# Kernel optimization log

Measured on AMD Instinct MI355X. Metric: run time of the kernel, lower is better.

The kernel has to match this reference:

```python
import jax, jax.numpy as jnp
import numpy as np

B, T, V, E, H, HD, L, K = 64, 512, 50000, 512, 512, 256, 2, 16
START, STOP, PAD = 13, 14, 15
NEG = -10000.0


def setup_inputs() -> dict:
    key = jax.random.key(0)
    ks = jax.random.split(key, 12)
    x = jax.random.randint(ks[0], (B, T), 0, V, dtype=jnp.int32)
    emb_table = jax.random.normal(ks[1], (V, E), jnp.float32) * 0.1
    w_ih = jax.random.normal(ks[2], (L, 2, 4 * HD, E), jnp.float32) * 0.05
    w_hh = jax.random.normal(ks[3], (L, 2, 4 * HD, HD), jnp.float32) * 0.05
    b_ih = jax.random.normal(ks[4], (L, 2, 4 * HD), jnp.float32) * 0.05
    b_hh = jax.random.normal(ks[5], (L, 2, 4 * HD), jnp.float32) * 0.05
    h0 = jax.random.normal(ks[6], (2 * L, B, HD), jnp.float32)
    c0 = jax.random.normal(ks[7], (2 * L, B, HD), jnp.float32)
    w_out = jax.random.normal(ks[8], (K, H), jnp.float32) * 0.05
    b_out = jax.random.normal(ks[9], (K,), jnp.float32) * 0.05
    t = jax.random.normal(ks[10], (K, K), jnp.float32)
    # replicate the in-place edits (order matters: pad overrides stop/start crossings)
    t = t.at[START, :].set(NEG)
    t = t.at[:, STOP].set(NEG)
    t = t.at[PAD, :].set(0.0)
    t = t.at[:, PAD].set(0.0)
    return {"x": x, "seq_len": T, "emb_table": emb_table, "w_ih": w_ih,
            "w_hh": w_hh, "b_ih": b_ih, "b_hh": b_hh, "h0": h0, "c0": c0,
            "w_out": w_out, "b_out": b_out, "transition": t}


def _lstm_dir(xs, h0, c0, Wih, Whh, b):
    # xs: [B, T, in]; single-direction LSTM, torch gate order (i, f, g, o)
    def step(carry, x_t):
        h, c = carry
        gates = x_t @ Wih.T + h @ Whh.T + b  # [B, 4*HD]
        i, f, g, o = jnp.split(gates, 4, axis=-1)
        c = jax.nn.sigmoid(f) * c + jax.nn.sigmoid(i) * jnp.tanh(g)
        h = jax.nn.sigmoid(o) * jnp.tanh(c)
        return (h, c), h
    _, hs = jax.lax.scan(step, (h0, c0), jnp.swapaxes(xs, 0, 1))  # [T, B, HD]
    return jnp.swapaxes(hs, 0, 1)


def _log_exp_sum(vec):
    # faithful to the original: per-row max over last dim, but sum of exp over ALL elements
    m = jnp.max(vec, axis=-1)
    return m + jnp.log(jnp.sum(jnp.exp(vec - m[..., None])))


def reference(x, seq_len, emb_table, w_ih, w_hh, b_ih, b_hh, h0, c0, w_out, b_out, transition):
    out = emb_table[x]  # [B, T, E]
    for l in range(L):
        fwd = _lstm_dir(out, h0[2 * l], c0[2 * l], w_ih[l, 0], w_hh[l, 0], b_ih[l, 0] + b_hh[l, 0])
        bwd = _lstm_dir(out[:, ::-1], h0[2 * l + 1], c0[2 * l + 1], w_ih[l, 1], w_hh[l, 1], b_ih[l, 1] + b_hh[l, 1])[:, ::-1]
        out = jnp.concatenate([fwd, bwd], axis=-1)  # [B, T, H]
    tag_scores = out @ w_out.T + b_out  # [B, T, K]

    # CRF forward algorithm (vectorized form of the nested time/tag loops)
    alpha0 = jnp.full((B, K), NEG, dtype=tag_scores.dtype).at[:, START].set(0.0)

    def crf_step(alpha, feat_t):  # feat_t: [B, K]
        vec = alpha[:, None, :] + feat_t[:, :, None] + transition[None, :, :]  # [B, Knext, Kprev]
        m = jnp.max(vec, axis=-1)  # [B, Knext]
        # original log_exp_sum sums exp over the whole [B, Kprev] slice per next_tag
        s = jnp.sum(jnp.exp(vec - m[..., None]), axis=(0, 2))  # [Knext]
        return m + jnp.log(s)[None, :], None

    alpha, _ = jax.lax.scan(crf_step, alpha0, jnp.swapaxes(tag_scores, 0, 1))
    terminal = alpha + transition[STOP][None, :]
    forward_score = _log_exp_sum(terminal)  # [B]
    return tag_scores, forward_score
```

## Files before the change

### kernel.cpp

```cpp
#include <hip/hip_runtime.h>

#define B_ 64
#define T_ 512
#define E_ 512
#define HD_ 256
#define H_ 512
#define K_ 16
#define NEG_ (-10000.0f)
#define START_ 13
#define STOP_ 14

typedef unsigned int u32;
using half8  = __attribute__((ext_vector_type(8))) _Float16;
using f32x4  = __attribute__((ext_vector_type(4))) float;
using half2v = __attribute__((ext_vector_type(2))) _Float16;

__device__ __forceinline__ int dot4i8(u32 a, u32 b, int c) {
#if __has_builtin(__builtin_amdgcn_sdot4)
    return __builtin_amdgcn_sdot4((int)a, (int)b, c, false);
#else
    int r = c;
#pragma unroll
    for (int i = 0; i < 4; ++i) {
        int xa = ((int)a << (24 - 8 * i)) >> 24;
        int xb = ((int)b << (24 - 8 * i)) >> 24;
        r += xa * xb;
    }
    return r;
#endif
}
__device__ __forceinline__ int dotq(uint4 w, uint4 h, int a) {
    a = dot4i8(w.x, h.x, a); a = dot4i8(w.y, h.y, a);
    a = dot4i8(w.z, h.z, a); a = dot4i8(w.w, h.w, a);
    return a;
}
__device__ __forceinline__ float sigm(float x) { return 1.f / (1.f + __expf(-x)); }
__device__ __forceinline__ float tanh_f(float x) {
    float a = fabsf(x);
    float e = __expf(-2.f * a);
    float t = (1.f - e) / (1.f + e);
    return x < 0.f ? -t : t;
}

__global__ void cvt_f16_k(const float* __restrict__ src, _Float16* __restrict__ dst, int n4) {
    int i = blockIdx.x * blockDim.x + threadIdx.x;
    if (i < n4) {
        float4 v = ((const float4*)src)[i];
        half2v a; a.x = (_Float16)v.x; a.y = (_Float16)v.y;
        half2v b; b.x = (_Float16)v.z; b.y = (_Float16)v.w;
        ((u32*)dst)[2 * i]     = __builtin_bit_cast(u32, a);
        ((u32*)dst)[2 * i + 1] = __builtin_bit_cast(u32, b);
    }
}
__global__ void bias_sum_k(const float* __restrict__ bih, const float* __restrict__ bhh,
                           float* __restrict__ bs) {
    int i = blockIdx.x * blockDim.x + threadIdx.x;
    if (i < 4096) bs[i] = bih[i] + bhh[i];
}

__global__ void quant_whh_k(const float* __restrict__ whh,
                            u32* __restrict__ wq,
                            float* __restrict__ dqw) {
    const int row = blockIdx.x, lane = threadIdx.x;
    const float4 v = ((const float4*)(whh + (size_t)row * 256))[lane];
    float m = fmaxf(fmaxf(fabsf(v.x), fabsf(v.y)), fmaxf(fabsf(v.z), fabsf(v.w)));
#pragma unroll
    for (int off = 32; off >= 1; off >>= 1) m = fmaxf(m, __shfl_xor(m, off, 64));
    m = fmaxf(m, 1e-8f);
    const float s = 127.f / m;
    int b0 = ((int)rintf(v.x * s)) & 255;
    int b1 = ((int)rintf(v.y * s)) & 255;
    int b2 = ((int)rintf(v.z * s)) & 255;
    int b3 = ((int)rintf(v.w * s)) & 255;
    wq[(size_t)row * 64 + lane] = (u32)(b0 | (b1 << 8) | (b2 << 16) | (b3 << 24));
    if (lane == 0) dqw[row] = m / (127.f * 127.f);
}

__global__ void embed_k(const int* __restrict__ x, const float* __restrict__ emb,
                        _Float16* __restrict__ xe) {
    int m = blockIdx.x;
    int row = x[m];
    int c = threadIdx.x * 4;
    float4 v = *(const float4*)(emb + (size_t)row * E_ + c);
    half2v p0; p0.x = (_Float16)v.x; p0.y = (_Float16)v.y;
    half2v p1; p1.x = (_Float16)v.z; p1.y = (_Float16)v.w;
    u32* dst = (u32*)(xe + (size_t)m * E_) + threadIdx.x * 2;
    dst[0] = __builtin_bit_cast(u32, p0);
    dst[1] = __builtin_bit_cast(u32, p1);
}

__global__ __launch_bounds__(256) void gemm_bt(const _Float16* __restrict__ A,
                                               const _Float16* __restrict__ Bw,
                                               const float* __restrict__ bsum,
                                               _Float16* __restrict__ C,
                                               int M, int N, int Kd) {
    __shared__ __align__(16) _Float16 As[128 * 64];
    __shared__ __align__(16) _Float16 Bs[128 * 64];
    const int nTn = N >> 7;
    const int tm = blockIdx.x / nTn, tn = blockIdx.x % nTn;
    const int tid = threadIdx.x;
    const int lane = tid & 63, wave = tid >> 6;
    const int wr = wave >> 1, wc = wave & 1;
    f32x4 acc[4][4];
#pragma unroll
    for (int i = 0; i < 4; ++i)
#pragma unroll
        for (int j = 0; j < 4; ++j) acc[i][j] = f32x4{0.f, 0.f, 0.f, 0.f};
    const int lr = lane & 15, lk = (lane >> 4) * 8;

    for (int k0 = 0; k0 < Kd; k0 += 64) {
#pragma unroll
        for (int r = 0; r < 4; ++r) {
            int c = r * 256 + tid;
            const _Float16* srcA = A + (size_t)(tm * 128 + (c >> 3)) * Kd + k0 + (c & 7) * 8;
            const _Float16* srcB = Bw + (size_t)(tn * 128 + (c >> 3)) * Kd + k0 + (c & 7) * 8;
            _Float16* dA = &As[(size_t)(r * 256 + wave * 64) * 8];
            _Float16* dB = &Bs[(size_t)(r * 256 + wave * 64) * 8];
            __builtin_amdgcn_global_load_lds((const __attribute__((address_space(1))) void*)srcA,
                                             (__attribute__((address_space(3))) void*)dA, 16, 0, 0);
            __builtin_amdgcn_global_load_lds((const __attribute__((address_space(1))) void*)srcB,
                                             (__attribute__((address_space(3))) void*)dB, 16, 0, 0);
        }
        __syncthreads();
#pragma unroll
        for (int kk = 0; kk < 2; ++kk) {
            half8 av[4], bv[4];
#pragma unroll
            for (int i = 0; i < 4; ++i)
                av[i] = *(const half8*)&As[(wr * 64 + i * 16 + lr) * 64 + kk * 32 + lk];
#pragma unroll
            for (int j = 0; j < 4; ++j)
                bv[j] = *(const half8*)&Bs[(wc * 64 + j * 16 + lr) * 64 + kk * 32 + lk];
#pragma unroll
            for (int i = 0; i < 4; ++i)
#pragma unroll
                for (int j = 0; j < 4; ++j)
                    acc[i][j] = __builtin_amdgcn_mfma_f32_16x16x32_f16(av[i], bv[j], acc[i][j], 0, 0, 0);
        }
        __syncthreads();
    }
    const int mq = (lane >> 4) * 4;
#pragma unroll
    for (int i = 0; i < 4; ++i)
#pragma unroll
        for (int j = 0; j < 4; ++j) {
            int m0 = tm * 128 + wr * 64 + i * 16 + mq;
            int n0 = tn * 128 + wc * 64 + j * 16 + lr;
            float bv = bsum[n0];
#pragma unroll
            for (int q = 0; q < 4; ++q)
                C[(size_t)(m0 + q) * N + n0] = (_Float16)(acc[i][j][q] + bv);
        }
}

__global__ __attribute__((amdgpu_flat_work_group_size(512, 512), amdgpu_waves_per_eu(2, 2)))
void lstm_layer_k(
    const u32* __restrict__ wq,
    const float* __restrict__ dqw,
    const float* __restrict__ h0,
    const float* __restrict__ c0,
    const _Float16* __restrict__ Z,
    _Float16* __restrict__ Hout) {
    __shared__ __align__(16) u32 hbuf[2][64];
    __shared__ float g_sh[1024];
    __shared__ float m0sh;
    const int tid = threadIdx.x;
    const int b = blockIdx.x >> 1, dir = blockIdx.x & 1;
    const int R0 = tid, R1 = tid + 512;

    const uint4* w4 = (const uint4*)(wq + (size_t)dir * 1024 * 64);
    uint4 wa[16], wb[16];
#pragma unroll
    for (int i = 0; i < 16; ++i) wa[i] = w4[(size_t)R0 * 16 + i];
#pragma unroll
    for (int i = 0; i < 16; ++i) wb[i] = w4[(size_t)R1 * 16 + i];
#pragma unroll
    for (int i = 0; i < 16; ++i) {
        asm volatile("" : "+v"(wa[i].x), "+v"(wa[i].y), "+v"(wa[i].z), "+v"(wa[i].w));
        asm volatile("" : "+v"(wb[i].x), "+v"(wb[i].y), "+v"(wb[i].z), "+v"(wb[i].w));
    }
    const float dq0 = dqw[dir * 1024 + R0];
    const float dq1 = dqw[dir * 1024 + R1];

    float c = 0.f;
    if (tid < 256) c = c0[(size_t)dir * B_ * HD_ + b * HD_ + tid];
    if (tid < 64) {
        float4 hv = ((const float4*)(h0 + (size_t)dir * B_ * HD_ + (size_t)b * HD_))[tid];
        float am = fmaxf(fmaxf(fabsf(hv.x), fabsf(hv.y)), fmaxf(fabsf(hv.z), fabsf(hv.w)));
#pragma unroll
        for (int off = 32; off >= 1; off >>= 1) am = fmaxf(am, __shfl_xor(am, off, 64));
        am = fmaxf(am, 1e-6f);
        float sc = 127.f / am;
        int q0 = ((int)rintf(hv.x * sc)) & 255, q1 = ((int)rintf(hv.y * sc)) & 255;
        int q2 = ((int)rintf(hv.z * sc)) & 255, q3 = ((int)rintf(hv.w * sc)) & 255;
        hbuf[0][tid] = (u32)(q0 | (q1 << 8) | (q2 << 16) | (q3 << 24));
        if (tid == 0) m0sh = am;
    }
    const _Float16* Zr = Z + (size_t)b * T_ * 2048 + dir * 1024;
    const int t0 = dir ? (T_ - 1) : 0;
    float z0 = (float)Zr[(size_t)t0 * 2048 + R0];
    float z1 = (float)Zr[(size_t)t0 * 2048 + R1];
    __syncthreads();
    const float m0v = m0sh;

    for (int s = 0; s < T_; ++s) {
        const int t = dir ? (T_ - 1 - s) : s;
        float zn0 = 0.f, zn1 = 0.f;
        if (s + 1 < T_) {
            const int tn = dir ? (t - 1) : (t + 1);
            zn0 = (float)Zr[(size_t)tn * 2048 + R0];
            zn1 = (float)Zr[(size_t)tn * 2048 + R1];
        }
        const uint4* hb = (const uint4*)&hbuf[s & 1][0];
        int a0 = 0, a1 = 0;
#pragma unroll
        for (int i = 0; i < 16; ++i) {
            uint4 hv = hb[i];
            a0 = dotq(wa[i], hv, a0);
            a1 = dotq(wb[i], hv, a1);
        }
        const float sc = (s == 0) ? m0v : 1.f;
        g_sh[R0] = (float)a0 * (dq0 * sc) + z0;
        g_sh[R1] = (float)a1 * (dq1 * sc) + z1;
        z0 = zn0; z1 = zn1;
        __syncthreads();
        if (tid < 256) {
            float gi = g_sh[tid], gf = g_sh[tid + 256];
            float gg = g_sh[tid + 512], go = g_sh[tid + 768];
            c = sigm(gf) * c + sigm(gi) * tanh_f(gg);
            float h = sigm(go) * tanh_f(c);
            Hout[(size_t)(b * T_ + t) * H_ + dir * HD_ + tid] = (_Float16)h;
            ((signed char*)&hbuf[(s + 1) & 1][0])[tid] = (signed char)(int)rintf(h * 127.f);
        }
        __syncthreads();
    }
}

__global__ __launch_bounds__(256) void tag_k(const _Float16* __restrict__ Hs,
                                             const float* __restrict__ wout,
                                             const float* __restrict__ bout,
                                             float* __restrict__ out) {
    const int tid = threadIdx.x;
    const int mi = tid >> 4, kk = tid & 15;
    const int m = blockIdx.x * 16 + mi;
    const uint4* hrow = (const uint4*)(Hs + (size_t)m * H_);
    const float4* wrow = (const float4*)(wout + (size_t)kk * H_);
    float acc = 0.f;
#pragma unroll 8
    for (int i = 0; i < 64; ++i) {
        uint4 hv = hrow[i];
        float4 w0 = wrow[2 * i], w1 = wrow[2 * i + 1];
        half2v p0 = __builtin_bit_cast(half2v, hv.x), p1 = __builtin_bit_cast(half2v, hv.y);
        half2v p2 = __builtin_bit_cast(half2v, hv.z), p3 = __builtin_bit_cast(half2v, hv.w);
        acc += (float)p0.x * w0.x + (float)p0.y * w0.y + (float)p1.x * w0.z + (float)p1.y * w0.w
             + (float)p2.x * w1.x + (float)p2.y * w1.y + (float)p3.x * w1.z + (float)p3.y * w1.w;
    }
    out[(size_t)m * K_ + kk] = acc + bout[kk];
}

__global__ __launch_bounds__(1024) void crf_k(const float* __restrict__ tag,
                                              const float* __restrict__ trans,
                                              float* __restrict__ out) {
    __shared__ float albuf[2][64][17];
    const int tid = threadIdx.x;
    const int kn = tid >> 6, b = tid & 63;
    float trow[16];
#pragma unroll
    for (int kp = 0; kp < 16; ++kp) trow[kp] = trans[kn * 16 + kp];
    albuf[0][b][kn] = (kn == START_) ? 0.f : NEG_;
    __syncthreads();
    int cur = 0;
    for (int t = 0; t < T_; ++t) {
        const float feat = tag[(size_t)(b * T_ + t) * K_ + kn];
        float v[16];
        float m = -3.4e38f;
#pragma unroll
        for (int kp = 0; kp < 16; ++kp) {
            v[kp] = albuf[cur][b][kp] + trow[kp];
            m = fmaxf(m, v[kp]);
        }
        float sm = 0.f;
#pragma unroll
        for (int kp = 0; kp < 16; ++kp) sm += __expf(v[kp] - m);
#pragma unroll
        for (int off = 32; off >= 1; off >>= 1) sm += __shfl_xor(sm, off, 64);
        albuf[cur ^ 1][b][kn] = feat + m + __logf(sm);
        __syncthreads();
        cur ^= 1;
    }
    const float term = albuf[cur][b][kn] + trans[STOP_ * 16 + kn];
    albuf[cur ^ 1][b][kn] = term;
    __syncthreads();
    if (tid < 64) {
        float mb = -3.4e38f;
#pragma unroll
        for (int k2 = 0; k2 < 16; ++k2) mb = fmaxf(mb, albuf[cur ^ 1][tid][k2]);
        float p = 0.f;
#pragma unroll
        for (int k2 = 0; k2 < 16; ++k2) p += __expf(albuf[cur ^ 1][tid][k2] - mb);
#pragma unroll
        for (int off = 32; off >= 1; off >>= 1) p += __shfl_xor(p, off, 64);
        out[(size_t)B_ * T_ * K_ + tid] = mb + __logf(p);
    }
}

extern "C" void kernel_launch(void* const* d_in, const int* in_sizes, int n_in,
                              void* d_out, int out_size, void* d_ws, size_t ws_size,
                              hipStream_t stream) {
    const int*   x     = (const int*)d_in[0];
    const float* emb   = (const float*)d_in[2];
    const float* w_ih  = (const float*)d_in[3];
    const float* w_hh  = (const float*)d_in[4];
    const float* b_ih  = (const float*)d_in[5];
    const float* b_hh  = (const float*)d_in[6];
    const float* h0    = (const float*)d_in[7];
    const float* c0    = (const float*)d_in[8];
    const float* w_out = (const float*)d_in[9];
    const float* b_out = (const float*)d_in[10];
    const float* trans = (const float*)d_in[11];
    float* out = (float*)d_out;

    char* ws = (char*)d_ws;
    u32*      wq    = (u32*)ws;
    float*    dqw   = (float*)(ws + ((size_t)1 << 20));
    _Float16* wih16 = (_Float16*)(ws + ((size_t)2 << 20));
    float*    bsum  = (float*)(ws + ((size_t)6 << 20));
    _Float16* xe    = (_Float16*)(ws + ((size_t)7 << 20));
    _Float16* Zb    = (_Float16*)(ws + ((size_t)39 << 20));
    _Float16* H0b   = (_Float16*)(ws + ((size_t)167 << 20));
    if (ws_size < ((size_t)199 << 20)) return;

    quant_whh_k<<<4096, 64, 0, stream>>>(w_hh, wq, dqw);
    cvt_f16_k<<<2048, 256, 0, stream>>>(w_ih, wih16, 2097152 / 4);
    bias_sum_k<<<16, 256, 0, stream>>>(b_ih, b_hh, bsum);
    embed_k<<<B_ * T_, 128, 0, stream>>>(x, emb, xe);

    gemm_bt<<<(32768 / 128) * (2048 / 128), 256, 0, stream>>>(xe, wih16, bsum, Zb, 32768, 2048, 512);
    lstm_layer_k<<<128, 512, 0, stream>>>(wq, dqw, h0, c0, Zb, H0b);
    gemm_bt<<<(32768 / 128) * (2048 / 128), 256, 0, stream>>>(H0b, wih16 + (size_t)2048 * 512, bsum + 2048, Zb, 32768, 2048, 512);
    lstm_layer_k<<<128, 512, 0, stream>>>(wq + (size_t)2048 * 64, dqw + 2048,
                                          h0 + 2 * B_ * HD_, c0 + 2 * B_ * HD_, Zb, xe );
    tag_k<<<32768 / 16, 256, 0, stream>>>(xe, w_out, b_out, out);
    crf_k<<<1, 1024, 0, stream>>>(out, trans, out);
}
```

Measured before the change: 1.946 ms.

## Compute all four gates per thread to drop shared-memory gate exchange and barrier

The LSTM recurrence kernel now runs 256 threads per block. Each thread holds the int8 weight rows for all four gates (i, f, g, o) of one hidden unit in registers. This removes the g_sh shared-memory gate buffer and one of the two __syncthreads per timestep, and keeps all threads active during the cell update. The h vector is loaded from LDS once per step, and split accumulators give extra ILP. In exchange each thread needs about 256 VGPRs for weights, forcing one wave per EU, with a risk of spills or lower latency hiding.

```diff
diff --git a/kernel.cpp b/kernel.cpp
--- a/kernel.cpp
+++ b/kernel.cpp
@@ -153,7 +153,7 @@
         }
 }
 
-__global__ __attribute__((amdgpu_flat_work_group_size(512, 512), amdgpu_waves_per_eu(2, 2)))
+__global__ __attribute__((amdgpu_flat_work_group_size(256, 256), amdgpu_waves_per_eu(1, 1)))
 void lstm_layer_k(
     const u32* __restrict__ wq,
     const float* __restrict__ dqw,
@@ -162,28 +162,32 @@
     const _Float16* __restrict__ Z,
     _Float16* __restrict__ Hout) {
     __shared__ __align__(16) u32 hbuf[2][64];
-    __shared__ float g_sh[1024];
     __shared__ float m0sh;
     const int tid = threadIdx.x;
     const int b = blockIdx.x >> 1, dir = blockIdx.x & 1;
-    const int R0 = tid, R1 = tid + 512;
 
     const uint4* w4 = (const uint4*)(wq + (size_t)dir * 1024 * 64);
-    uint4 wa[16], wb[16];
-#pragma unroll
-    for (int i = 0; i < 16; ++i) wa[i] = w4[(size_t)R0 * 16 + i];
-#pragma unroll
-    for (int i = 0; i < 16; ++i) wb[i] = w4[(size_t)R1 * 16 + i];
+    uint4 w0[16], w1[16], w2[16], w3[16];
 #pragma unroll
     for (int i = 0; i < 16; ++i) {
-        asm volatile("" : "+v"(wa[i].x), "+v"(wa[i].y), "+v"(wa[i].z), "+v"(wa[i].w));
-        asm volatile("" : "+v"(wb[i].x), "+v"(wb[i].y), "+v"(wb[i].z), "+v"(wb[i].w));
-    }
-    const float dq0 = dqw[dir * 1024 + R0];
-    const float dq1 = dqw[dir * 1024 + R1];
-
-    float c = 0.f;
-    if (tid < 256) c = c0[(size_t)dir * B_ * HD_ + b * HD_ + tid];
+        w0[i] = w4[(size_t)(0 * 256 + tid) * 16 + i];
+        w1[i] = w4[(size_t)(1 * 256 + tid) * 16 + i];
+        w2[i] = w4[(size_t)(2 * 256 + tid) * 16 + i];
+        w3[i] = w4[(size_t)(3 * 256 + tid) * 16 + i];
+    }
+#pragma unroll
+    for (int i = 0; i < 16; ++i) {
+        asm("" : "+v"(w0[i].x), "+v"(w0[i].y), "+v"(w0[i].z), "+v"(w0[i].w));
+        asm("" : "+v"(w1[i].x), "+v"(w1[i].y), "+v"(w1[i].z), "+v"(w1[i].w));
+        asm("" : "+v"(w2[i].x), "+v"(w2[i].y), "+v"(w2[i].z), "+v"(w2[i].w));
+        asm("" : "+v"(w3[i].x), "+v"(w3[i].y), "+v"(w3[i].z), "+v"(w3[i].w));
+    }
+    const float dq0 = dqw[dir * 1024 + 0 * 256 + tid];
+    const float dq1 = dqw[dir * 1024 + 1 * 256 + tid];
+    const float dq2 = dqw[dir * 1024 + 2 * 256 + tid];
+    const float dq3 = dqw[dir * 1024 + 3 * 256 + tid];
+
+    float c = c0[(size_t)dir * B_ * HD_ + b * HD_ + tid];
     if (tid < 64) {
         float4 hv = ((const float4*)(h0 + (size_t)dir * B_ * HD_ + (size_t)b * HD_))[tid];
         float am = fmaxf(fmaxf(fabsf(hv.x), fabsf(hv.y)), fmaxf(fabsf(hv.z), fabsf(hv.w)));
@@ -198,40 +202,46 @@
     }
     const _Float16* Zr = Z + (size_t)b * T_ * 2048 + dir * 1024;
     const int t0 = dir ? (T_ - 1) : 0;
-    float z0 = (float)Zr[(size_t)t0 * 2048 + R0];
-    float z1 = (float)Zr[(size_t)t0 * 2048 + R1];
+    float z0 = (float)Zr[(size_t)t0 * 2048 + 0 * 256 + tid];
+    float z1 = (float)Zr[(size_t)t0 * 2048 + 1 * 256 + tid];
+    float z2 = (float)Zr[(size_t)t0 * 2048 + 2 * 256 + tid];
+    float z3 = (float)Zr[(size_t)t0 * 2048 + 3 * 256 + tid];
     __syncthreads();
     const float m0v = m0sh;
+    float dqa = dq0 * m0v, dqb = dq1 * m0v, dqc = dq2 * m0v, dqd = dq3 * m0v;
 
     for (int s = 0; s < T_; ++s) {
         const int t = dir ? (T_ - 1 - s) : s;
-        float zn0 = 0.f, zn1 = 0.f;
+        float zn0 = 0.f, zn1 = 0.f, zn2 = 0.f, zn3 = 0.f;
         if (s + 1 < T_) {
             const int tn = dir ? (t - 1) : (t + 1);
-            zn0 = (float)Zr[(size_t)tn * 2048 + R0];
-            zn1 = (float)Zr[(size_t)tn * 2048 + R1];
+            zn0 = (float)Zr[(size_t)tn * 2048 + 0 * 256 + tid];
+            zn1 = (float)Zr[(size_t)tn * 2048 + 1 * 256 + tid];
+            zn2 = (float)Zr[(size_t)tn * 2048 + 2 * 256 + tid];
+            zn3 = (float)Zr[(size_t)tn * 2048 + 3 * 256 + tid];
         }
         const uint4* hb = (const uint4*)&hbuf[s & 1][0];
-        int a0 = 0, a1 = 0;
-#pragma unroll
-        for (int i = 0; i < 16; ++i) {
-            uint4 hv = hb[i];
-            a0 = dotq(wa[i], hv, a0);
-            a1 = dotq(wb[i], hv, a1);
-        }
-        const float sc = (s == 0) ? m0v : 1.f;
-        g_sh[R0] = (float)a0 * (dq0 * sc) + z0;
-        g_sh[R1] = (float)a1 * (dq1 * sc) + z1;
-        z0 = zn0; z1 = zn1;
-        __syncthreads();
-        if (tid < 256) {
-            float gi = g_sh[tid], gf = g_sh[tid + 256];
-            float gg = g_sh[tid + 512], go = g_sh[tid + 768];
-            c = sigm(gf) * c + sigm(gi) * tanh_f(gg);
-            float h = sigm(go) * tanh_f(c);
-            Hout[(size_t)(b * T_ + t) * H_ + dir * HD_ + tid] = (_Float16)h;
-            ((signed char*)&hbuf[(s + 1) & 1][0])[tid] = (signed char)(int)rintf(h * 127.f);
-        }
+        uint4 hv[16];
+#pragma unroll
+        for (int i = 0; i < 16; ++i) hv[i] = hb[i];
+        int p0 = 0, p1 = 0, p2 = 0, p3 = 0, q0 = 0, q1 = 0, q2 = 0, q3 = 0;
+#pragma unroll
+        for (int i = 0; i < 16; i += 2) {
+            p0 = dotq(w0[i], hv[i], p0); q0 = dotq(w0[i + 1], hv[i + 1], q0);
+            p1 = dotq(w1[i], hv[i], p1); q1 = dotq(w1[i + 1], hv[i + 1], q1);
+            p2 = dotq(w2[i], hv[i], p2); q2 = dotq(w2[i + 1], hv[i + 1], q2);
+            p3 = dotq(w3[i], hv[i], p3); q3 = dotq(w3[i + 1], hv[i + 1], q3);
+        }
+        const float gi = (float)(p0 + q0) * dqa + z0;
+        const float gf = (float)(p1 + q1) * dqb + z1;
+        const float gg = (float)(p2 + q2) * dqc + z2;
+        const float go = (float)(p3 + q3) * dqd + z3;
+        c = sigm(gf) * c + sigm(gi) * tanh_f(gg);
+        const float h = sigm(go) * tanh_f(c);
+        Hout[(size_t)(b * T_ + t) * H_ + dir * HD_ + tid] = (_Float16)h;
+        ((signed char*)&hbuf[(s + 1) & 1][0])[tid] = (signed char)(int)rintf(h * 127.f);
+        if (s == 0) { dqa = dq0; dqb = dq1; dqc = dq2; dqd = dq3; }
+        z0 = zn0; z1 = zn1; z2 = zn2; z3 = zn3;
         __syncthreads();
     }
 }
@@ -336,9 +346,9 @@
     embed_k<<<B_ * T_, 128, 0, stream>>>(x, emb, xe);
 
     gemm_bt<<<(32768 / 128) * (2048 / 128), 256, 0, stream>>>(xe, wih16, bsum, Zb, 32768, 2048, 512);
-    lstm_layer_k<<<128, 512, 0, stream>>>(wq, dqw, h0, c0, Zb, H0b);
+    lstm_layer_k<<<128, 256, 0, stream>>>(wq, dqw, h0, c0, Zb, H0b);
     gemm_bt<<<(32768 / 128) * (2048 / 128), 256, 0, stream>>>(H0b, wih16 + (size_t)2048 * 512, bsum + 2048, Zb, 32768, 2048, 512);
-    lstm_layer_k<<<128, 512, 0, stream>>>(wq + (size_t)2048 * 64, dqw + 2048,
+    lstm_layer_k<<<128, 256, 0, stream>>>(wq + (size_t)2048 * 64, dqw + 2048,
                                           h0 + 2 * B_ * HD_, c0 + 2 * B_ * HD_, Zb, xe );
     tag_k<<<32768 / 16, 256, 0, stream>>>(xe, w_out, b_out, out);
     crf_k<<<1, 1024, 0, stream>>>(out, trans, out);
```

Result: slower. 2.351 ms (+20.8%).
